# Optimization experiments

Measured on AMD Instinct MI355X. Metric: run time of the kernel, lower is better.

Reference implementation:

```python
import jax, jax.numpy as jnp
import numpy as np
from jax import lax

VOCAB, EMBED, HIDDEN, TAGS, PAD = 50000, 512, 512, 20, 0
B, T = 64, 512


def _lstm_layer(xs, W_ih, W_hh, b_ih, b_hh):
    # xs: (B, T, D) -> hs: (B, T, H). PyTorch ifgo gate order.
    Bm = xs.shape[0]
    H = W_hh.shape[1]
    h0 = jnp.zeros((Bm, H), xs.dtype)
    c0 = jnp.zeros((Bm, H), xs.dtype)
    # precompute input projections for all timesteps: (T, B, 4H)
    xproj = jnp.einsum('btd,gd->tbg', xs, W_ih) + b_ih

    def step(carry, xp_t):
        h, c = carry
        gates = xp_t + h @ W_hh.T + b_hh
        i, f, g, o = jnp.split(gates, 4, axis=-1)
        i = jax.nn.sigmoid(i)
        f = jax.nn.sigmoid(f)
        g = jnp.tanh(g)
        o = jax.nn.sigmoid(o)
        c = f * c + i * g
        h = o * jnp.tanh(c)
        return (h, c), h

    (_, _), hs = lax.scan(step, (h0, c0), xproj)
    return hs.transpose(1, 0, 2)  # (B, T, H)


def setup_inputs() -> dict:
    key = jax.random.key(0)
    ks = jax.random.split(key, 12)
    s = 0.05
    emb = jax.random.normal(ks[0], (VOCAB, EMBED), jnp.float32) * s
    emb = emb.at[PAD].set(0.0)  # padding_idx row is zero
    W_ih0 = jax.random.normal(ks[1], (4 * HIDDEN, EMBED), jnp.float32) * s
    W_hh0 = jax.random.normal(ks[2], (4 * HIDDEN, HIDDEN), jnp.float32) * s
    b_ih0 = jax.random.normal(ks[3], (4 * HIDDEN,), jnp.float32) * s
    b_hh0 = jax.random.normal(ks[4], (4 * HIDDEN,), jnp.float32) * s
    W_ih1 = jax.random.normal(ks[5], (4 * HIDDEN, HIDDEN), jnp.float32) * s
    W_hh1 = jax.random.normal(ks[6], (4 * HIDDEN, HIDDEN), jnp.float32) * s
    b_ih1 = jax.random.normal(ks[7], (4 * HIDDEN,), jnp.float32) * s
    b_hh1 = jax.random.normal(ks[8], (4 * HIDDEN,), jnp.float32) * s
    W_out = jax.random.normal(ks[9], (TAGS, HIDDEN), jnp.float32) * s
    b_out = jax.random.normal(ks[10], (TAGS,), jnp.float32) * s
    x = jax.random.randint(ks[11], (B, T), 0, VOCAB, dtype=jnp.int64 if jax.config.jax_enable_x64 else jnp.int32)
    return dict(x=x, emb=emb, W_ih0=W_ih0, W_hh0=W_hh0, b_ih0=b_ih0, b_hh0=b_hh0,
                W_ih1=W_ih1, W_hh1=W_hh1, b_ih1=b_ih1, b_hh1=b_hh1,
                W_out=W_out, b_out=b_out)


def reference(x, emb, W_ih0, W_hh0, b_ih0, b_hh0, W_ih1, W_hh1, b_ih1, b_hh1, W_out, b_out):
    batch_size, max_len = x.shape
    lens = max_len - jnp.sum(x == PAD, axis=-1)  # (B,)
    h = emb[x]                                    # (B, T, E) embedding lookup
    h = _lstm_layer(h, W_ih0, W_hh0, b_ih0, b_hh0)
    h = _lstm_layer(h, W_ih1, W_hh1, b_ih1, b_hh1)
    last = h[jnp.arange(batch_size), lens - 1, :]  # length-masked last-step gather
    return last @ W_out.T + b_out                  # (B, TAGS)
```

## Files before the change

kernel.cpp:

```cpp
#include <hip/hip_runtime.h>
#include <hip/hip_bf16.h>
#include <stdint.h>

#define B_    64
#define T_    512
#define H_    512
#define G_    2048
#define TAGS_ 20

typedef __hip_bfloat16 bf16;
typedef __bf16 bf16x8 __attribute__((ext_vector_type(8)));
typedef float  f32x4  __attribute__((ext_vector_type(4)));
typedef unsigned int u32;
typedef u32 u32x4 __attribute__((ext_vector_type(4)));
typedef u32 u32x2 __attribute__((ext_vector_type(2)));

__device__ __forceinline__ float sigmoidf_(float x) { return 1.0f / (1.0f + __expf(-x)); }
__device__ __forceinline__ float tanhf_(float x)    { return 1.0f - 2.0f / (__expf(2.0f * x) + 1.0f); }


__global__ void k_zero(uint32_t* __restrict__ p, int n) {
    for (int i = blockIdx.x * blockDim.x + threadIdx.x; i < n; i += gridDim.x * blockDim.x)
        p[i] = 0u;
}

__global__ void k_addb(const float* __restrict__ a, const float* __restrict__ b,
                       float* __restrict__ o, int n) {
    for (int i = blockIdx.x * blockDim.x + threadIdx.x; i < n; i += gridDim.x * blockDim.x)
        o[i] = a[i] + b[i];
}

__global__ __launch_bounds__(256) void k_lens(const int* __restrict__ x, int* __restrict__ lens) {
    int b = blockIdx.x;
    int cnt = 0;
    for (int tpos = threadIdx.x; tpos < T_; tpos += 256)
        cnt += (x[(size_t)b * T_ + tpos] == 0) ? 1 : 0;
    #pragma unroll
    for (int off = 32; off; off >>= 1) cnt += __shfl_xor(cnt, off);
    __shared__ int tot;
    if (threadIdx.x == 0) tot = 0;
    __syncthreads();
    if ((threadIdx.x & 63) == 0) atomicAdd(&tot, cnt);
    __syncthreads();
    if (threadIdx.x == 0) lens[b] = T_ - tot;
}

__global__ __launch_bounds__(256) void k_gather(const int* __restrict__ x,
                                                const float* __restrict__ emb,
                                                char* __restrict__ Epk) {
    const int t = blockIdx.x, m = blockIdx.y;
    __shared__ int tok[16];
    if (threadIdx.x < 16) tok[threadIdx.x] = x[(size_t)(m * 16 + threadIdx.x) * T_ + t];
    __syncthreads();
    char* base = Epk + ((size_t)(t * 4 + m)) * 16384;
    for (int task = threadIdx.x; task < 1024; task += 256) {
        int f = task >> 6, lane = task & 63;
        int r = lane & 15, kqi = lane >> 4;
        const float* src = emb + (size_t)tok[r] * H_ + f * 32 + kqi * 8;
        bf16 tmp[8];
        #pragma unroll
        for (int e = 0; e < 8; ++e) tmp[e] = __float2bfloat16(src[e]);
        *reinterpret_cast<f32x4*>(base + f * 1024 + lane * 16) =
            *reinterpret_cast<f32x4*>(tmp);
    }
}

__global__ __launch_bounds__(256) void k_pack(const float* __restrict__ Wih0, const float* __restrict__ Whh0,
                                              const float* __restrict__ Wih1, const float* __restrict__ Whh1,
                                              bf16* __restrict__ Wp) {
    const int s = blockIdx.x, q = blockIdx.y, l = blockIdx.z;
    const float* Wx = l ? Wih1 : Wih0;
    const float* Wh = l ? Whh1 : Whh0;
    bf16* base = Wp + (size_t)(l * 32 + s) * 65536;
    for (int u = threadIdx.x; u < 2048; u += 256) {
        int kc = u >> 6, lane = u & 63;
        int row = q * H_ + s * 16 + (lane & 15);
        int col = (kc & 15) * 32 + (lane >> 4) * 8;
        const float* src = ((kc < 16) ? Wx : Wh) + (size_t)row * H_ + col;
        bf16* dst = base + ((size_t)(q * 32 + kc) * 64 + lane) * 8;
        #pragma unroll
        for (int e = 0; e < 8; ++e) dst[e] = __float2bfloat16(src[e]);
    }
}


#define WAITALL()                                                            \
    asm volatile("s_waitcnt vmcnt(0)" ::: "memory");                         \
    __builtin_amdgcn_sched_barrier(0);

#define ISSUE_CH(CA, CB, base)                                               \
    _Pragma("unroll")                                                        \
    for (int i = 0; i < 4; ++i) {                                            \
        const char* pa_ = (base) + (2 * (q * 4 + i) + (kqi >> 1)) * 1024     \
                          + (qa * 16 + row) * 16;                            \
        asm volatile("global_load_dwordx4 %0, %2, off sc0 sc1\n\t"           \
                     "global_load_dwordx4 %1, %3, off sc0 sc1"               \
                     : "=v"(CA[i]), "=v"(CB[i])                              \
                     : "v"(pa_), "v"(pa_ + 256));                            \
    }

#define CHECK8(CA, CB, sq, okv)                                              \
    { okv = 1;                                                               \
      _Pragma("unroll")                                                      \
      for (int i = 0; i < 4; ++i)                                            \
          okv &= (CA[i].z == (u32)(sq)) & (CB[i].z == (u32)(sq)); }

#define STAGE_CH(CA, CB, fbase)                                              \
    _Pragma("unroll")                                                        \
    for (int i = 0; i < 4; ++i) {                                            \
        u32x4 fr_ = u32x4{CA[i].x, CA[i].y, CB[i].x, CB[i].y};               \
        stagev[(size_t)((fbase) + q * 4 + i) * 64 + lane] =                  \
            __builtin_bit_cast(f32x4, fr_);                                  \
    }

#define ISSUE16L(arr, basep)                                                 \
    _Pragma("unroll")                                                        \
    for (int kc = 0; kc < 16; ++kc) {                                        \
        asm volatile("global_load_dwordx4 %0, %1, off"                       \
                     : "=v"(arr[kc]) : "v"((basep) + kc * 1024));            \
    }

#define MFMA16_REG(arr, woff)                                                \
    _Pragma("unroll")                                                        \
    for (int kc = 0; kc < 16; ++kc) {                                        \
        f32x4 wf = wldsv[(size_t)(q * 32 + (woff) + kc) * 64 + lane];        \
        acc[kc & 3] = __builtin_amdgcn_mfma_f32_16x16x32_bf16(               \
            __builtin_bit_cast(bf16x8, arr[kc]),                             \
            __builtin_bit_cast(bf16x8, wf), acc[kc & 3], 0, 0, 0);           \
    }

#define MFMA16_S(soff, woff)                                                 \
    _Pragma("unroll")                                                        \
    for (int kc = 0; kc < 16; ++kc) {                                        \
        f32x4 af = stagev[(size_t)((soff) + kc) * 64 + lane];                \
        f32x4 wf = wldsv[(size_t)(q * 32 + (woff) + kc) * 64 + lane];        \
        acc[kc & 3] = __builtin_amdgcn_mfma_f32_16x16x32_bf16(               \
            __builtin_bit_cast(bf16x8, af),                                  \
            __builtin_bit_cast(bf16x8, wf), acc[kc & 3], 0, 0, 0);           \
    }

__global__ __launch_bounds__(256, 1) void k_lstm(
    const bf16* __restrict__ Wp, const char* __restrict__ Epk,
    const float* __restrict__ bias0, const float* __restrict__ bias1,
    char* __restrict__ h0ring, char* __restrict__ h1ring,
    int* __restrict__ fx, float* __restrict__ last1, const int* __restrict__ lens)
{
    extern __shared__ char smem[];
    f32x4* wldsv  = (f32x4*)smem;
    f32x4* stagev = (f32x4*)(smem + 131072);

    const int bid   = blockIdx.x;
    const int g     = bid & 7;
    const int s     = bid >> 3;
    const int layer = g >> 2;
    const int m     = g & 3;
    const int tid   = threadIdx.x;
    const int lane  = tid & 63;
    const int q     = tid >> 6;
    const int kqi   = lane >> 4;
    const int row   = lane & 15;
    const int qa    = (kqi & 1) * 2;

    float (*glds)[16][20] = layer ? (float (*)[16][20])(smem + 131072)
                                  : (float (*)[16][20])(smem + 131072 + 16384);
    bf16* hlds = layer ? (bf16*)(smem + 131072 + 5120)
                       : (bf16*)(smem + 131072 + 16384 + 5120);

    {
        const f32x4* wsrc = (const f32x4*)(Wp + (size_t)(layer * 32 + s) * 65536);
        for (int i = tid; i < 8192; i += 256) wldsv[i] = wsrc[i];
    }

    const int eb   = tid >> 4;
    const int ej   = tid & 15;
    const int brow = m * 16 + eb;
    const int jcol = s * 16 + ej;
    float c_reg = 0.f;
    const float* bias = layer ? bias1 : bias0;
    const float bi0 = bias[0 * H_ + jcol];
    const float bi1 = bias[1 * H_ + jcol];
    const float bi2 = bias[2 * H_ + jcol];
    const float bi3 = bias[3 * H_ + jcol];
    int target = lens[brow] - 1;
    if (target < 0) target = T_ - 1;

    int* flagp = fx + m * 32;

    char* grp0 = h0ring + (size_t)m * 8 * 32768;
    char* grp1 = h1ring + (size_t)m * 8 * 32768;
    char* mygrp = layer ? grp1 : grp0;
    const int rb = (lane >> 4) * 4;
    const int l15 = lane & 15;

    __syncthreads();

    for (int tt = 0; tt < T_; ++tt) {
        f32x4 acc[4];
        #pragma unroll
        for (int i = 0; i < 4; ++i) acc[i] = f32x4{0.f, 0.f, 0.f, 0.f};
        const int slot_w = tt & 7;
        const int slot_r = (tt - 1) & 7;

        if (layer == 0) {
            f32x4 xreg[16];
            const char* xp = Epk + ((size_t)(tt * 4 + m)) * 16384 + lane * 16;
            ISSUE16L(xreg, xp)
            const char* hbase = grp0 + slot_r * 32768;
            u32x4 ca[4], cb[4];
            ISSUE_CH(ca, cb, hbase)
            WAITALL()
            MFMA16_REG(xreg, 0)
            int ok; CHECK8(ca, cb, tt, ok)
            int gd = 0;
            while (!__all(ok)) {
                if (++gd > (1 << 16)) break;
                ISSUE_CH(ca, cb, hbase)
                WAITALL()
                CHECK8(ca, cb, tt, ok)
            }
            __builtin_amdgcn_sched_barrier(0);
            STAGE_CH(ca, cb, 0)
            __syncthreads();
            MFMA16_S(0, 16)
        } else {
            const char* xbase = grp0 + slot_w * 32768;
            const char* hbase = grp1 + slot_r * 32768;
            u32x4 xa[4], xb[4], ha[4], hb[4];
            ISSUE_CH(xa, xb, xbase)
            ISSUE_CH(ha, hb, hbase)
            WAITALL()
            int okx, okh;
            CHECK8(xa, xb, tt + 1, okx)
            CHECK8(ha, hb, tt, okh)
            int gd = 0;
            while (!__all(okx & okh)) {
                if (++gd > (1 << 16)) break;
                ISSUE_CH(xa, xb, xbase)
                ISSUE_CH(ha, hb, hbase)
                WAITALL()
                CHECK8(xa, xb, tt + 1, okx)
                CHECK8(ha, hb, tt, okh)
            }
            __builtin_amdgcn_sched_barrier(0);
            STAGE_CH(xa, xb, 0)
            STAGE_CH(ha, hb, 16)
            __syncthreads();
            if (tid == 0) {
                int fv = tt + 1;
                asm volatile("global_store_dword %0, %1, off sc0 sc1" :: "v"(flagp), "v"(fv) : "memory");
            }
            MFMA16_S(0, 0)
            MFMA16_S(16, 16)
            __syncthreads();
        }

        f32x4 gsum = (acc[0] + acc[1]) + (acc[2] + acc[3]);

        *reinterpret_cast<f32x4*>(&glds[q][l15][rb]) = gsum;
        __syncthreads();

        float gi = sigmoidf_(glds[0][ej][eb] + bi0);
        float gf = sigmoidf_(glds[1][ej][eb] + bi1);
        float gg = tanhf_  (glds[2][ej][eb] + bi2);
        float go = sigmoidf_(glds[3][ej][eb] + bi3);
        c_reg = gf * c_reg + gi * gg;
        float hn = go * tanhf_(c_reg);

        hlds[eb * 16 + ej] = __float2bfloat16(hn);
        if (layer == 1 && tt == target)
            last1[(size_t)brow * H_ + jcol] = hn;
        __syncthreads();

        if (layer == 0 && tid < 64 && tt >= 8) {
            int gd2 = 0;
            while (true) {
                int v;
                asm volatile("global_load_dword %0, %1, off sc0 sc1\n\ts_waitcnt vmcnt(0)"
                             : "=v"(v) : "v"(flagp) : "memory");
                if (v >= tt - 7) break;
                if (++gd2 > (1 << 16)) break;
                __builtin_amdgcn_s_sleep(2);
            }
            __builtin_amdgcn_sched_barrier(0);
        }

        if (tid < 64) {
            int prow = tid & 15, pq = tid >> 4;
            u32x2 d = *reinterpret_cast<const u32x2*>(&hlds[prow * 16 + pq * 4]);
            u32x4 ch = u32x4{d.x, d.y, (u32)(tt + 1), 0u};
            char* dst = mygrp + slot_w * 32768 + s * 1024 + tid * 16;
            asm volatile("global_store_dwordx4 %0, %1, off sc0 sc1"
                         :: "v"(dst), "v"(__builtin_bit_cast(f32x4, ch)) : "memory");
        }
    }
}

__global__ __launch_bounds__(64) void k_out(const float* __restrict__ last1,
                                            const float* __restrict__ Wout,
                                            const float* __restrict__ bout,
                                            float* __restrict__ out) {
    int b = blockIdx.x, tg = blockIdx.y, lane = threadIdx.x;
    float sum = 0.f;
    for (int d = lane; d < H_; d += 64)
        sum += last1[(size_t)b * H_ + d] * Wout[(size_t)tg * H_ + d];
    #pragma unroll
    for (int off = 32; off; off >>= 1) sum += __shfl_xor(sum, off);
    if (lane == 0) out[b * TAGS_ + tg] = sum + bout[tg];
}


extern "C" void kernel_launch(void* const* d_in, const int* in_sizes, int n_in,
                              void* d_out, int out_size, void* d_ws, size_t ws_size,
                              hipStream_t stream)
{
    const int*   x    = (const int*)  d_in[0];
    const float* emb  = (const float*)d_in[1];
    const float* Wih0 = (const float*)d_in[2];
    const float* Whh0 = (const float*)d_in[3];
    const float* bih0 = (const float*)d_in[4];
    const float* bhh0 = (const float*)d_in[5];
    const float* Wih1 = (const float*)d_in[6];
    const float* Whh1 = (const float*)d_in[7];
    const float* bih1 = (const float*)d_in[8];
    const float* bhh1 = (const float*)d_in[9];
    const float* Wout = (const float*)d_in[10];
    const float* bout = (const float*)d_in[11];
    float* out = (float*)d_out;

    char* p = (char*)d_ws;
    char* Epk  = p;         p += (size_t)T_ * 4 * 16384;
    bf16* Wp   = (bf16*)p;  p += (size_t)2 * 32 * 65536 * 2;
    float* bias0 = (float*)p; p += (size_t)G_ * 4;
    float* bias1 = (float*)p; p += (size_t)G_ * 4;
    char* zbase = p;
    char* h0ring = p; p += (size_t)4 * 8 * 32768;
    char* h1ring = p; p += (size_t)4 * 8 * 32768;
    int*  fx     = (int*)p;  p += 8 * 32 * 4;
    size_t zbytes = (size_t)(p - zbase);
    float* last1 = (float*)p; p += (size_t)B_ * H_ * 4;
    int* lens = (int*)p; p += 256;

    (void)hipFuncSetAttribute((const void*)k_lstm,
                              hipFuncAttributeMaxDynamicSharedMemorySize, 163840);

    k_zero<<<dim3(128), dim3(256), 0, stream>>>((uint32_t*)zbase, (int)(zbytes / 4));
    k_lens<<<dim3(B_), dim3(256), 0, stream>>>(x, lens);
    k_addb<<<dim3(8), dim3(256), 0, stream>>>(bih0, bhh0, bias0, G_);
    k_addb<<<dim3(8), dim3(256), 0, stream>>>(bih1, bhh1, bias1, G_);
    k_pack<<<dim3(32, 4, 2), dim3(256), 0, stream>>>(Wih0, Whh0, Wih1, Whh1, Wp);
    k_gather<<<dim3(T_, 4), dim3(256), 0, stream>>>(x, emb, Epk);

    k_lstm<<<dim3(256), dim3(256), 163840, stream>>>(Wp, Epk, bias0, bias1,
                                                     h0ring, h1ring, fx, last1, lens);

    k_out<<<dim3(B_, TAGS_), dim3(64), 0, stream>>>(last1, Wout, bout, out);
}
```

Before: 1.662 ms.

## Add agent-scope duplicate hidden-state ring for faster same-XCD polling

Each block now writes its hidden-state chunk to two rings: a local copy with sc0 only (agent/L2 scope) and the original system-coherent copy with sc0 sc1. Consumers poll the local copy first and fall back to the global copy only when the local read is stale. The intent is to cut cross-step handoff latency when producer and consumer share an L2. The cost is a second store per step, extra polling loads and a larger zeroed workspace. Whether blocks actually share an XCD depends on how the hardware schedules them.

```diff
diff --git a/kernel.cpp b/kernel.cpp
--- a/kernel.cpp
+++ b/kernel.cpp
@@ -88,13 +88,13 @@
     asm volatile("s_waitcnt vmcnt(0)" ::: "memory");                         \
     __builtin_amdgcn_sched_barrier(0);
 
-#define ISSUE_CH(CA, CB, base)                                               \
+#define ISSUE_CHF(CA, CB, base, SC)                                          \
     _Pragma("unroll")                                                        \
     for (int i = 0; i < 4; ++i) {                                            \
         const char* pa_ = (base) + (2 * (q * 4 + i) + (kqi >> 1)) * 1024     \
                           + (qa * 16 + row) * 16;                            \
-        asm volatile("global_load_dwordx4 %0, %2, off sc0 sc1\n\t"           \
-                     "global_load_dwordx4 %1, %3, off sc0 sc1"               \
+        asm volatile("global_load_dwordx4 %0, %2, off" SC "\n\t"             \
+                     "global_load_dwordx4 %1, %3, off" SC                    \
                      : "=v"(CA[i]), "=v"(CB[i])                              \
                      : "v"(pa_), "v"(pa_ + 256));                            \
     }
@@ -143,6 +143,7 @@
     const bf16* __restrict__ Wp, const char* __restrict__ Epk,
     const float* __restrict__ bias0, const float* __restrict__ bias1,
     char* __restrict__ h0ring, char* __restrict__ h1ring,
+    char* __restrict__ h0loc, char* __restrict__ h1loc,
     int* __restrict__ fx, float* __restrict__ last1, const int* __restrict__ lens)
 {
     extern __shared__ char smem[];
@@ -188,7 +189,10 @@
 
     char* grp0 = h0ring + (size_t)m * 8 * 32768;
     char* grp1 = h1ring + (size_t)m * 8 * 32768;
+    char* loc0 = h0loc + (size_t)m * 8 * 32768;
+    char* loc1 = h1loc + (size_t)m * 8 * 32768;
     char* mygrp = layer ? grp1 : grp0;
+    char* myloc = layer ? loc1 : loc0;
     const int rb = (lane >> 4) * 4;
     const int l15 = lane & 15;
 
@@ -205,29 +209,41 @@
             f32x4 xreg[16];
             const char* xp = Epk + ((size_t)(tt * 4 + m)) * 16384 + lane * 16;
             ISSUE16L(xreg, xp)
-            const char* hbase = grp0 + slot_r * 32768;
+            const char* hL = loc0 + slot_r * 32768;
+            const char* hG = grp0 + slot_r * 32768;
             u32x4 ca[4], cb[4];
-            ISSUE_CH(ca, cb, hbase)
+            ISSUE_CHF(ca, cb, hL, " sc0")
             WAITALL()
             MFMA16_REG(xreg, 0)
             int ok; CHECK8(ca, cb, tt, ok)
             int gd = 0;
             while (!__all(ok)) {
                 if (++gd > (1 << 16)) break;
-                ISSUE_CH(ca, cb, hbase)
+                u32x4 ga[4], gb[4];
+                ISSUE_CHF(ca, cb, hL, " sc0")
+                ISSUE_CHF(ga, gb, hG, " sc0 sc1")
                 WAITALL()
                 CHECK8(ca, cb, tt, ok)
+                if (!__all(ok)) {
+                    int ok2; CHECK8(ga, gb, tt, ok2)
+                    if (__all(ok2)) {
+                        #pragma unroll
+                        for (int i = 0; i < 4; ++i) { ca[i] = ga[i]; cb[i] = gb[i]; }
+                        ok = 1;
+                    }
+                }
             }
             __builtin_amdgcn_sched_barrier(0);
             STAGE_CH(ca, cb, 0)
             __syncthreads();
             MFMA16_S(0, 16)
         } else {
-            const char* xbase = grp0 + slot_w * 32768;
-            const char* hbase = grp1 + slot_r * 32768;
+            const char* xG = grp0 + slot_w * 32768;
+            const char* hL = loc1 + slot_r * 32768;
+            const char* hG = grp1 + slot_r * 32768;
             u32x4 xa[4], xb[4], ha[4], hb[4];
-            ISSUE_CH(xa, xb, xbase)
-            ISSUE_CH(ha, hb, hbase)
+            ISSUE_CHF(ha, hb, hL, " sc0")
+            ISSUE_CHF(xa, xb, xG, " sc0 sc1")
             WAITALL()
             int okx, okh;
             CHECK8(xa, xb, tt + 1, okx)
@@ -235,11 +251,26 @@
             int gd = 0;
             while (!__all(okx & okh)) {
                 if (++gd > (1 << 16)) break;
-                ISSUE_CH(xa, xb, xbase)
-                ISSUE_CH(ha, hb, hbase)
-                WAITALL()
-                CHECK8(xa, xb, tt + 1, okx)
-                CHECK8(ha, hb, tt, okh)
+                if (!__all(okh)) {
+                    u32x4 ga[4], gb[4];
+                    ISSUE_CHF(ha, hb, hL, " sc0")
+                    ISSUE_CHF(ga, gb, hG, " sc0 sc1")
+                    WAITALL()
+                    CHECK8(ha, hb, tt, okh)
+                    if (!__all(okh)) {
+                        int ok2; CHECK8(ga, gb, tt, ok2)
+                        if (__all(ok2)) {
+                            #pragma unroll
+                            for (int i = 0; i < 4; ++i) { ha[i] = ga[i]; hb[i] = gb[i]; }
+                            okh = 1;
+                        }
+                    }
+                }
+                if (!__all(okx)) {
+                    ISSUE_CHF(xa, xb, xG, " sc0 sc1")
+                    WAITALL()
+                    CHECK8(xa, xb, tt + 1, okx)
+                }
             }
             __builtin_amdgcn_sched_barrier(0);
             STAGE_CH(xa, xb, 0)
@@ -288,9 +319,13 @@
             int prow = tid & 15, pq = tid >> 4;
             u32x2 d = *reinterpret_cast<const u32x2*>(&hlds[prow * 16 + pq * 4]);
             u32x4 ch = u32x4{d.x, d.y, (u32)(tt + 1), 0u};
-            char* dst = mygrp + slot_w * 32768 + s * 1024 + tid * 16;
+            f32x4 chv = __builtin_bit_cast(f32x4, ch);
+            char* dstL = myloc + slot_w * 32768 + s * 1024 + tid * 16;
+            char* dstG = mygrp + slot_w * 32768 + s * 1024 + tid * 16;
+            asm volatile("global_store_dwordx4 %0, %1, off sc0"
+                         :: "v"(dstL), "v"(chv) : "memory");
             asm volatile("global_store_dwordx4 %0, %1, off sc0 sc1"
-                         :: "v"(dst), "v"(__builtin_bit_cast(f32x4, ch)) : "memory");
+                         :: "v"(dstG), "v"(chv) : "memory");
         }
     }
 }
@@ -335,6 +370,8 @@
     char* zbase = p;
     char* h0ring = p; p += (size_t)4 * 8 * 32768;
     char* h1ring = p; p += (size_t)4 * 8 * 32768;
+    char* h0loc  = p; p += (size_t)4 * 8 * 32768;
+    char* h1loc  = p; p += (size_t)4 * 8 * 32768;
     int*  fx     = (int*)p;  p += 8 * 32 * 4;
     size_t zbytes = (size_t)(p - zbase);
     float* last1 = (float*)p; p += (size_t)B_ * H_ * 4;
@@ -351,7 +388,8 @@
     k_gather<<<dim3(T_, 4), dim3(256), 0, stream>>>(x, emb, Epk);
 
     k_lstm<<<dim3(256), dim3(256), 163840, stream>>>(Wp, Epk, bias0, bias1,
-                                                     h0ring, h1ring, fx, last1, lens);
+                                                     h0ring, h1ring, h0loc, h1loc,
+                                                     fx, last1, lens);
 
     k_out<<<dim3(B_, TAGS_), dim3(64), 0, stream>>>(last1, Wout, bout, out);
 }
```

Result: faster. 1.468 ms (-11.7%).
